# Kernel optimization log

Hardware: AMD Instinct MI355X
Metric: run time of the kernel (lower is better)

Reference implementation:

```python
import jax, jax.numpy as jnp
import numpy as np

W = 0.5  # loss weight from __init__
EPS = 1e-14


def gradient_l2_loss(x):
    """Mean squared forward finite-difference along each spatial axis of (B,s,r,c)."""
    loss = 0.0
    for ax in (1, 2, 3):
        d = jnp.diff(x, axis=ax)
        loss = loss + jnp.mean(d * d)
    return loss


def setup_inputs() -> dict:
    key = jax.random.key(0)
    k1, k2 = jax.random.split(key)
    B, S, R, C = 2, 128, 128, 128
    L = jax.random.normal(k1, (B, 3, S, R, C), dtype=jnp.float32)
    U = jax.random.normal(k2, (B, 9, S, R, C), dtype=jnp.float32)
    return {"L": L, "U": U}


def reference(L, U):
    B, _, S, R, C = U.shape
    # torch.sort(L, dim=1, descending=True) -> indices[:,0] == argmax over the 3 eigenvalues
    idx0 = jnp.argmax(L, axis=1)  # (B,S,R,C) int
    # U channel layout U{row}_{col}: reshape to (B, col=3, row=3, S,R,C)
    Uview = U.reshape(B, 3, 3, S, R, C)
    idx = jnp.broadcast_to(idx0[:, None, None], (B, 3, 1, S, R, C))
    # faithful to original gather(dim=2)[:, :, 0]
    major = jnp.take_along_axis(Uview, idx, axis=2)[:, :, 0]  # (B,3,S,R,C)
    am = jnp.abs(major)
    den = jnp.sum(am * am, axis=1)  # (B,S,R,C)
    den = jnp.where(den < EPS, EPS, den)
    e1, e2, e3 = am[:, 0], am[:, 1], am[:, 2]
    CO = jnp.sqrt(0.5 * ((e1 - e2) ** 2 + (e2 - e3) ** 2 + (e3 - e1) ** 2) / den)
    CO_grad = 0.0
    for i in range(9):  # fixed small channel loop
        CO_grad = CO_grad + gradient_l2_loss(U[:, i])
    return (CO + CO_grad).mean() * W
```

## Files before the change

### kernel.cpp

```cpp
#include <hip/hip_runtime.h>

#define SS 128
#define RR 128
#define CC 128
#define EPSF 1e-14f

__global__ __launch_bounds__(256, 2) void scol_main(const float* __restrict__ L,
                                                    const float* __restrict__ U,
                                                    float4* __restrict__ part) {
    const int SRC = SS * RR * CC;

    int tid = threadIdx.x;
    int c4  = tid & 31;
    int row = blockIdx.x * 8 + (tid >> 5);
    int r   = row & (RR - 1);
    int sr  = row >> 7;
    int s   = sr & (SS - 1);
    int b   = sr >> 7;
    int c   = c4 << 2;

    int pos    = (row - b * (SS * RR)) * CC + c;
    int base_l = b * 3 * SRC + pos;
    int base_u = b * 9 * SRC + pos;

    bool  hr = (r < RR - 1), hs = (s < SS - 1), hc = (c4 < 31);
    float wr = hr ? 1.f : 0.f;
    float ws = hs ? 1.f : 0.f;
    float wc = hc ? 1.f : 0.f;
    int offr = hr ? CC : 0;
    int offs = hs ? RR * CC : 0;

    float4 l0 = *(const float4*)(L + base_l);
    float4 l1 = *(const float4*)(L + base_l + SRC);
    float4 l2 = *(const float4*)(L + base_l + 2 * SRC);

    float4 u[9], ur[9], us[9];
#pragma unroll
    for (int ch = 0; ch < 9; ++ch) {
        const float* p = U + base_u + ch * SRC;
        u[ch] = *(const float4*)(p);
    }
#pragma unroll
    for (int ch = 0; ch < 9; ++ch) {
        const float* p = U + base_u + ch * SRC;
        ur[ch] = *(const float4*)(p + offr);
        us[ch] = *(const float4*)(p + offs);
    }

    float L0[4] = {l0.x, l0.y, l0.z, l0.w};
    float L1[4] = {l1.x, l1.y, l1.z, l1.w};
    float L2[4] = {l2.x, l2.y, l2.z, l2.w};
    int idx[4];
#pragma unroll
    for (int j = 0; j < 4; ++j) {
        int id = 0;
        float best = L0[j];
        if (L1[j] > best) { best = L1[j]; id = 1; }
        if (L2[j] > best) { best = L2[j]; id = 2; }
        idx[j] = id;
    }

    float am[3][4];
#pragma unroll
    for (int g = 0; g < 3; ++g)
#pragma unroll
        for (int j = 0; j < 4; ++j) am[g][j] = 0.f;

    float a_dc = 0.f, t_dcb = 0.f, t_dr = 0.f, t_ds = 0.f;

#pragma unroll
    for (int ch = 0; ch < 9; ++ch) {
        float4 uu = u[ch];
        float uuv[4] = {uu.x, uu.y, uu.z, uu.w};
        int g = ch / 3, m = ch % 3;
#pragma unroll
        for (int j = 0; j < 4; ++j)
            if (idx[j] == m) am[g][j] = fabsf(uuv[j]);

        float d;
        d = uu.y - uu.x; a_dc += d * d;
        d = uu.z - uu.y; a_dc += d * d;
        d = uu.w - uu.z; a_dc += d * d;
        float un = __shfl_down(uu.x, 1);
        d = un - uu.w; t_dcb += d * d;

        float4 R4 = ur[ch];
        d = R4.x - uu.x; t_dr += d * d;
        d = R4.y - uu.y; t_dr += d * d;
        d = R4.z - uu.z; t_dr += d * d;
        d = R4.w - uu.w; t_dr += d * d;

        float4 S4 = us[ch];
        d = S4.x - uu.x; t_ds += d * d;
        d = S4.y - uu.y; t_ds += d * d;
        d = S4.z - uu.z; t_ds += d * d;
        d = S4.w - uu.w; t_ds += d * d;
    }
    a_dc += wc * t_dcb;
    float a_dr = wr * t_dr;
    float a_ds = ws * t_ds;

    float a_co = 0.f;
#pragma unroll
    for (int j = 0; j < 4; ++j) {
        float e1 = am[0][j], e2 = am[1][j], e3 = am[2][j];
        float den = e1 * e1 + e2 * e2 + e3 * e3;
        den = fmaxf(den, EPSF);
        float num = 0.5f * ((e1 - e2) * (e1 - e2) + (e2 - e3) * (e2 - e3) +
                            (e3 - e1) * (e3 - e1));
        a_co += sqrtf(num / den);
    }

#pragma unroll
    for (int off = 32; off > 0; off >>= 1) {
        a_co += __shfl_down(a_co, off);
        a_ds += __shfl_down(a_ds, off);
        a_dr += __shfl_down(a_dr, off);
        a_dc += __shfl_down(a_dc, off);
    }

    __shared__ float s_co[4], s_ds[4], s_dr[4], s_dc[4];
    int wid  = threadIdx.x >> 6;
    int lane = threadIdx.x & 63;
    if (lane == 0) {
        s_co[wid] = a_co; s_ds[wid] = a_ds;
        s_dr[wid] = a_dr; s_dc[wid] = a_dc;
    }
    __syncthreads();
    if (threadIdx.x == 0) {
        float t_co = 0.f, t_s = 0.f, t_r = 0.f, t_c = 0.f;
        for (int w = 0; w < 4; ++w) {
            t_co += s_co[w]; t_s += s_ds[w];
            t_r += s_dr[w]; t_c += s_dc[w];
        }
        part[blockIdx.x] = make_float4(t_co, t_s, t_r, t_c);
    }
}

__global__ __launch_bounds__(256) void scol_final(const float4* __restrict__ part,
                                                  float* __restrict__ out,
                                                  int nblk, int B) {
    double d_co = 0., d_ds = 0., d_dr = 0., d_dc = 0.;
    for (int i = threadIdx.x; i < nblk; i += blockDim.x) {
        float4 p = part[i];
        d_co += (double)p.x; d_ds += (double)p.y;
        d_dr += (double)p.z; d_dc += (double)p.w;
    }
#pragma unroll
    for (int off = 32; off > 0; off >>= 1) {
        d_co += __shfl_down(d_co, off);
        d_ds += __shfl_down(d_ds, off);
        d_dr += __shfl_down(d_dr, off);
        d_dc += __shfl_down(d_dc, off);
    }
    __shared__ double sh[4][4];
    int wid  = threadIdx.x >> 6;
    int lane = threadIdx.x & 63;
    if (lane == 0) {
        sh[wid][0] = d_co; sh[wid][1] = d_ds;
        sh[wid][2] = d_dr; sh[wid][3] = d_dc;
    }
    __syncthreads();
    if (threadIdx.x == 0) {
        double t_co = 0., t_ds = 0., t_dr = 0., t_dc = 0.;
        for (int w = 0; w < 4; ++w) {
            t_co += sh[w][0]; t_ds += sh[w][1];
            t_dr += sh[w][2]; t_dc += sh[w][3];
        }
        double nvox = (double)B * SS * RR * CC;
        double nds  = (double)B * (SS - 1) * RR * CC;
        double ndr  = (double)B * SS * (RR - 1) * CC;
        double ndc  = (double)B * SS * RR * (CC - 1);
        out[0] = (float)(0.5 * (t_co / nvox + t_ds / nds + t_dr / ndr + t_dc / ndc));
    }
}

extern "C" void kernel_launch(void* const* d_in, const int* in_sizes, int n_in,
                              void* d_out, int out_size, void* d_ws, size_t ws_size,
                              hipStream_t stream) {
    const float* L = (const float*)d_in[0];
    const float* U = (const float*)d_in[1];
    float* out = (float*)d_out;

    int B = in_sizes[1] / (9 * SS * RR * CC);
    int nrow = B * SS * RR;
    int blocks = nrow / 8;

    float4* part = (float4*)d_ws;

    hipLaunchKernelGGL(scol_main, dim3(blocks), dim3(256), 0, stream,
                       L, U, part);
    hipLaunchKernelGGL(scol_final, dim3(1), dim3(256), 0, stream,
                       part, out, blocks, B);
}
```

Measured before the change: 245.4 us.

## March each block along the slice axis, reusing the next-slice load as current

Each block now walks LS=8 consecutive slices instead of handling one row-slab. The next-slice values loaded for the s-direction difference are carried over in registers as the next iteration's current values. This removes one of the three per-channel U loads per voxel, cutting L2/HBM request traffic. The cost is 8x fewer blocks (4096 → 512 on this shape), less parallelism and more register pressure from the carried state, which could hurt latency hiding.

New measurement: 256.1 us. 4.4% more time.

```diff
diff --git a/kernel.cpp b/kernel.cpp
--- a/kernel.cpp
+++ b/kernel.cpp
@@ -3,112 +3,130 @@
 #define SS 128
 #define RR 128
 #define CC 128
+#define RC (RR * CC)
+#define LS 8
 #define EPSF 1e-14f
 
 __global__ __launch_bounds__(256, 2) void scol_main(const float* __restrict__ L,
                                                     const float* __restrict__ U,
-                                                    float4* __restrict__ part) {
-    const int SRC = SS * RR * CC;
-
-    int tid = threadIdx.x;
-    int c4  = tid & 31;
-    int row = blockIdx.x * 8 + (tid >> 5);
-    int r   = row & (RR - 1);
-    int sr  = row >> 7;
-    int s   = sr & (SS - 1);
-    int b   = sr >> 7;
-    int c   = c4 << 2;
-
-    int pos    = (row - b * (SS * RR)) * CC + c;
-    int base_l = b * 3 * SRC + pos;
-    int base_u = b * 9 * SRC + pos;
-
-    bool  hr = (r < RR - 1), hs = (s < SS - 1), hc = (c4 < 31);
+                                                    float4* __restrict__ part,
+                                                    int sChunks, int rChunks) {
+    const int SRC = SS * RC;
+
+    int tid  = threadIdx.x;
+    int c4   = tid & 31;
+    int rblk = tid >> 5;
+
+    int g   = blockIdx.x;
+    int sc  = g % sChunks;
+    int rc  = (g / sChunks) % rChunks;
+    int b   = g / (sChunks * rChunks);
+
+    int r  = rc * 8 + rblk;
+    int s0 = sc * LS;
+    int c  = c4 << 2;
+
+    bool  hr = (r < RR - 1), hc = (c4 < 31);
     float wr = hr ? 1.f : 0.f;
-    float ws = hs ? 1.f : 0.f;
     float wc = hc ? 1.f : 0.f;
     int offr = hr ? CC : 0;
-    int offs = hs ? RR * CC : 0;
-
-    float4 l0 = *(const float4*)(L + base_l);
-    float4 l1 = *(const float4*)(L + base_l + SRC);
-    float4 l2 = *(const float4*)(L + base_l + 2 * SRC);
-
-    float4 u[9], ur[9], us[9];
-#pragma unroll
-    for (int ch = 0; ch < 9; ++ch) {
-        const float* p = U + base_u + ch * SRC;
-        u[ch] = *(const float4*)(p);
-    }
-#pragma unroll
-    for (int ch = 0; ch < 9; ++ch) {
-        const float* p = U + base_u + ch * SRC;
-        ur[ch] = *(const float4*)(p + offr);
-        us[ch] = *(const float4*)(p + offs);
-    }
-
-    float L0[4] = {l0.x, l0.y, l0.z, l0.w};
-    float L1[4] = {l1.x, l1.y, l1.z, l1.w};
-    float L2[4] = {l2.x, l2.y, l2.z, l2.w};
-    int idx[4];
-#pragma unroll
-    for (int j = 0; j < 4; ++j) {
-        int id = 0;
-        float best = L0[j];
-        if (L1[j] > best) { best = L1[j]; id = 1; }
-        if (L2[j] > best) { best = L2[j]; id = 2; }
-        idx[j] = id;
-    }
-
-    float am[3][4];
-#pragma unroll
-    for (int g = 0; g < 3; ++g)
-#pragma unroll
-        for (int j = 0; j < 4; ++j) am[g][j] = 0.f;
-
-    float a_dc = 0.f, t_dcb = 0.f, t_dr = 0.f, t_ds = 0.f;
-
-#pragma unroll
-    for (int ch = 0; ch < 9; ++ch) {
-        float4 uu = u[ch];
-        float uuv[4] = {uu.x, uu.y, uu.z, uu.w};
-        int g = ch / 3, m = ch % 3;
-#pragma unroll
-        for (int j = 0; j < 4; ++j)
-            if (idx[j] == m) am[g][j] = fabsf(uuv[j]);
-
-        float d;
-        d = uu.y - uu.x; a_dc += d * d;
-        d = uu.z - uu.y; a_dc += d * d;
-        d = uu.w - uu.z; a_dc += d * d;
-        float un = __shfl_down(uu.x, 1);
-        d = un - uu.w; t_dcb += d * d;
-
-        float4 R4 = ur[ch];
-        d = R4.x - uu.x; t_dr += d * d;
-        d = R4.y - uu.y; t_dr += d * d;
-        d = R4.z - uu.z; t_dr += d * d;
-        d = R4.w - uu.w; t_dr += d * d;
-
-        float4 S4 = us[ch];
-        d = S4.x - uu.x; t_ds += d * d;
-        d = S4.y - uu.y; t_ds += d * d;
-        d = S4.z - uu.z; t_ds += d * d;
-        d = S4.w - uu.w; t_ds += d * d;
-    }
-    a_dc += wc * t_dcb;
-    float a_dr = wr * t_dr;
-    float a_ds = ws * t_ds;
-
-    float a_co = 0.f;
-#pragma unroll
-    for (int j = 0; j < 4; ++j) {
-        float e1 = am[0][j], e2 = am[1][j], e3 = am[2][j];
-        float den = e1 * e1 + e2 * e2 + e3 * e3;
-        den = fmaxf(den, EPSF);
-        float num = 0.5f * ((e1 - e2) * (e1 - e2) + (e2 - e3) * (e2 - e3) +
-                            (e3 - e1) * (e3 - e1));
-        a_co += sqrtf(num / den);
+
+    int pos    = (s0 * RR + r) * CC + c;
+    int base_l = b * 3 * SRC;
+    int base_u = b * 9 * SRC;
+
+    float4 ucur[9];
+#pragma unroll
+    for (int ch = 0; ch < 9; ++ch)
+        ucur[ch] = *(const float4*)(U + base_u + ch * SRC + pos);
+
+    float a_co = 0.f, a_ds = 0.f, a_dr = 0.f, a_dc = 0.f;
+
+#pragma unroll 2
+    for (int i = 0; i < LS; ++i) {
+        int s = s0 + i;
+        bool  hs  = (s < SS - 1);
+        float wsf = hs ? 1.f : 0.f;
+        int offn  = hs ? RC : 0;
+
+        float4 l0 = *(const float4*)(L + base_l + pos);
+        float4 l1 = *(const float4*)(L + base_l + SRC + pos);
+        float4 l2 = *(const float4*)(L + base_l + 2 * SRC + pos);
+
+        float4 urv[9], unx[9];
+#pragma unroll
+        for (int ch = 0; ch < 9; ++ch) {
+            const float* p = U + base_u + ch * SRC + pos;
+            urv[ch] = *(const float4*)(p + offr);
+            unx[ch] = *(const float4*)(p + offn);
+        }
+
+        float L0[4] = {l0.x, l0.y, l0.z, l0.w};
+        float L1[4] = {l1.x, l1.y, l1.z, l1.w};
+        float L2[4] = {l2.x, l2.y, l2.z, l2.w};
+        int idx[4];
+#pragma unroll
+        for (int j = 0; j < 4; ++j) {
+            int id = 0;
+            float best = L0[j];
+            if (L1[j] > best) { best = L1[j]; id = 1; }
+            if (L2[j] > best) { best = L2[j]; id = 2; }
+            idx[j] = id;
+        }
+
+        float am[3][4];
+#pragma unroll
+        for (int gi = 0; gi < 3; ++gi)
+#pragma unroll
+            for (int j = 0; j < 4; ++j) am[gi][j] = 0.f;
+
+        float t_dcb = 0.f, t_dr = 0.f, t_ds = 0.f;
+
+#pragma unroll
+        for (int ch = 0; ch < 9; ++ch) {
+            float4 uu = ucur[ch];
+            float uuv[4] = {uu.x, uu.y, uu.z, uu.w};
+            int gi = ch / 3, m = ch % 3;
+#pragma unroll
+            for (int j = 0; j < 4; ++j)
+                if (idx[j] == m) am[gi][j] = fabsf(uuv[j]);
+
+            float d;
+            d = uu.y - uu.x; a_dc += d * d;
+            d = uu.z - uu.y; a_dc += d * d;
+            d = uu.w - uu.z; a_dc += d * d;
+            float un1 = __shfl_down(uu.x, 1);
+            d = un1 - uu.w; t_dcb += d * d;
+
+            float4 R4 = urv[ch];
+            d = R4.x - uu.x; t_dr += d * d;
+            d = R4.y - uu.y; t_dr += d * d;
+            d = R4.z - uu.z; t_dr += d * d;
+            d = R4.w - uu.w; t_dr += d * d;
+
+            float4 S4 = unx[ch];
+            d = S4.x - uu.x; t_ds += d * d;
+            d = S4.y - uu.y; t_ds += d * d;
+            d = S4.z - uu.z; t_ds += d * d;
+            d = S4.w - uu.w; t_ds += d * d;
+
+            ucur[ch] = S4;
+        }
+        a_dc += wc * t_dcb;
+        a_dr += wr * t_dr;
+        a_ds += wsf * t_ds;
+
+#pragma unroll
+        for (int j = 0; j < 4; ++j) {
+            float e1 = am[0][j], e2 = am[1][j], e3 = am[2][j];
+            float den = e1 * e1 + e2 * e2 + e3 * e3;
+            den = fmaxf(den, EPSF);
+            float num = 0.5f * ((e1 - e2) * (e1 - e2) + (e2 - e3) * (e2 - e3) +
+                                (e3 - e1) * (e3 - e1));
+            a_co += sqrtf(num / den);
+        }
+
+        pos += RC;
     }
 
 #pragma unroll
@@ -183,13 +201,14 @@
     float* out = (float*)d_out;
 
     int B = in_sizes[1] / (9 * SS * RR * CC);
-    int nrow = B * SS * RR;
-    int blocks = nrow / 8;
+    int sChunks = SS / LS;
+    int rChunks = RR / 8;
+    int blocks  = B * sChunks * rChunks;
 
     float4* part = (float4*)d_ws;
 
     hipLaunchKernelGGL(scol_main, dim3(blocks), dim3(256), 0, stream,
-                       L, U, part);
+                       L, U, part, sChunks, rChunks);
     hipLaunchKernelGGL(scol_final, dim3(1), dim3(256), 0, stream,
                        part, out, blocks, B);
 }
```
